# Kernel optimization log

Hardware: AMD Instinct MI355X
Metric: run time of the kernel (lower is better)

Reference implementation:

```python
import jax, jax.numpy as jnp
import numpy as np

B, S, N, U, E, L = 32, 32, 128, 64, 2, 2
N_STEPS = 3
NUM_CLASSES = 5


def setup_inputs() -> dict:
    key = jax.random.key(0)
    ks = jax.random.split(key, 10)
    input_seq = jax.random.normal(ks[0], (B, S, N * U), dtype=jnp.float32)
    seq_lengths = jax.random.randint(ks[1], (B,), 0, S)
    # per-edge-type adjacency, scaled ~row-stochastic for numerical sanity
    adjacency_matrix = jax.random.uniform(ks[2], (B, E, N, N), dtype=jnp.float32) / N
    sc = 1.0 / np.sqrt(U)
    W_msg = jax.random.normal(ks[3], (L, E, U, U), dtype=jnp.float32) * sc
    b_msg = jnp.zeros((L, U), dtype=jnp.float32)
    Wg = jax.random.normal(ks[4], (L, 3, U, U), dtype=jnp.float32) * sc  # gates from aggregated messages
    Ug = jax.random.normal(ks[5], (L, 3, U, U), dtype=jnp.float32) * sc  # gates from hidden state
    bg = jnp.zeros((L, 3, U), dtype=jnp.float32)
    fc_w = jax.random.normal(ks[6], (U, NUM_CLASSES), dtype=jnp.float32) * sc
    fc_b = jnp.zeros((NUM_CLASSES,), dtype=jnp.float32)
    return {
        "input_seq": input_seq, "seq_lengths": seq_lengths,
        "adjacency_matrix": adjacency_matrix,
        "W_msg": W_msg, "b_msg": b_msg, "Wg": Wg, "Ug": Ug, "bg": bg,
        "fc_w": fc_w, "fc_b": fc_b,
    }


def _ggnn_layer(h, A, W_msg_l, b_msg_l, Wg_l, Ug_l, bg_l):
    # h: [S,B,N,U], A: [B,E,N,N] (shared across timesteps)
    for _ in range(N_STEPS):
        # typed message passing: sum_e A_e @ h @ W_e
        a = jnp.einsum('benm,sbmu,euv->sbnv', A, h, W_msg_l) + b_msg_l
        g_a = jnp.einsum('sbnu,guv->gsbnv', a, Wg_l)  # [3,S,B,N,U]
        z = jax.nn.sigmoid(g_a[0] + h @ Ug_l[0] + bg_l[0])
        r = jax.nn.sigmoid(g_a[1] + h @ Ug_l[1] + bg_l[1])
        c = jnp.tanh(g_a[2] + (r * h) @ Ug_l[2] + bg_l[2])
        h = (1.0 - z) * h + z * c
    return h


def reference(input_seq, seq_lengths, adjacency_matrix, W_msg, b_msg, Wg, Ug, bg, fc_w, fc_b):
    # encoder: hidden state is NOT carried across timesteps in the original
    # (cell is called with current input only), so timesteps are vectorized.
    cur = input_seq.reshape(B, S, N, U).transpose(1, 0, 2, 3)  # [S,B,N,U]
    for l in range(L):
        cur = _ggnn_layer(cur, adjacency_matrix, W_msg[l], b_msg[l], Wg[l], Ug[l], bg[l])
    out = cur.transpose(1, 0, 2, 3)  # [B,S,N,U]
    idx = jnp.clip(seq_lengths - 1, 0, S - 1)
    last = out[jnp.arange(B), idx]  # [B,N,U] (last relevant timestep)
    # dropout is identity in eval mode
    logits = jax.nn.relu(last) @ fc_w + fc_b  # [B,N,C]
    return jnp.max(logits, axis=1)  # [B,C]
```

## Files before the change

### kernel.cpp

```cpp
#include <hip/hip_runtime.h>

#define B 32
#define S 32
#define N 128
#define U 64
#define E 2
#define NCLS 5


__device__ __forceinline__ float sigmoid_f(float x) {
    return __fdividef(1.f, 1.f + __expf(-x));
}
__device__ __forceinline__ float tanh_f(float x) {
    float t = __expf(-2.f * fabsf(x));
    float y = __fdividef(1.f - t, 1.f + t);
    return copysignf(y, x);
}
__device__ __forceinline__ float bcast(float v, int u) {
    return __uint_as_float(__builtin_amdgcn_readlane(__float_as_uint(v), u));
}

template <int FIRST, int LAST>
__global__ __launch_bounds__(512, 2) void k_step(
    const float* __restrict__ x, const int* __restrict__ lens,
    const float* __restrict__ hin, float* __restrict__ hout,
    const float* __restrict__ A, const float* __restrict__ Wmsg,
    const float* __restrict__ bmsg, const float* __restrict__ Wg,
    const float* __restrict__ Ug, const float* __restrict__ bg,
    const float* __restrict__ fcw, float* __restrict__ partial, int l) {
    __shared__ float sred[4][2][2][2][64];
    __shared__ float avred[4][2][2][64];
    __shared__ float gred[4][2][3][2][64];
    __shared__ float c2red[4][2][2][64];
    __shared__ float red[4 * NCLS];
    int tid = threadIdx.x;
    int wave = tid >> 6, lane = tid & 63;
    int g = wave & 3;
    int k = wave >> 2;
    int b = blockIdx.x >> 4;
    int j = blockIdx.x & 15;
    int n0 = __builtin_amdgcn_readfirstlane(j * 8 + g * 2);
    int u0 = __builtin_amdgcn_readfirstlane(k * 32);
    int m0 = __builtin_amdgcn_readfirstlane(k * 64);

    const float* __restrict__ hsrc;
    if (FIRST) {
        int idx = lens[b] - 1;
        idx = idx < 0 ? 0 : (idx > S - 1 ? S - 1 : idx);
        hsrc = x + (size_t)(b * S + idx) * N * U;
    } else {
        hsrc = hin + (size_t)b * N * U;
    }

    float hv0 = hsrc[(n0 + 0) * U + lane];
    float hv1 = hsrc[(n0 + 1) * U + lane];

    float s00 = 0.f, s01 = 0.f, s10 = 0.f, s11 = 0.f;
    {
        const float4* A00 = (const float4*)(A + (((size_t)b * E + 0) * N + n0 + 0) * N + m0);
        const float4* A10 = (const float4*)(A + (((size_t)b * E + 0) * N + n0 + 1) * N + m0);
        const float4* A01 = (const float4*)(A + (((size_t)b * E + 1) * N + n0 + 0) * N + m0);
        const float4* A11 = (const float4*)(A + (((size_t)b * E + 1) * N + n0 + 1) * N + m0);
#pragma unroll 8
        for (int m4 = 0; m4 < 16; ++m4) {
            float4 a00 = A00[m4], a10 = A10[m4], a01 = A01[m4], a11 = A11[m4];
            float q0 = hsrc[(m0 + m4 * 4 + 0) * U + lane];
            float q1 = hsrc[(m0 + m4 * 4 + 1) * U + lane];
            float q2 = hsrc[(m0 + m4 * 4 + 2) * U + lane];
            float q3 = hsrc[(m0 + m4 * 4 + 3) * U + lane];
            s00 = fmaf(a00.x, q0, s00); s00 = fmaf(a00.y, q1, s00);
            s00 = fmaf(a00.z, q2, s00); s00 = fmaf(a00.w, q3, s00);
            s10 = fmaf(a10.x, q0, s10); s10 = fmaf(a10.y, q1, s10);
            s10 = fmaf(a10.z, q2, s10); s10 = fmaf(a10.w, q3, s10);
            s01 = fmaf(a01.x, q0, s01); s01 = fmaf(a01.y, q1, s01);
            s01 = fmaf(a01.z, q2, s01); s01 = fmaf(a01.w, q3, s01);
            s11 = fmaf(a11.x, q0, s11); s11 = fmaf(a11.y, q1, s11);
            s11 = fmaf(a11.z, q2, s11); s11 = fmaf(a11.w, q3, s11);
        }
    }
    sred[g][k][0][0][lane] = s00;
    sred[g][k][0][1][lane] = s01;
    sred[g][k][1][0][lane] = s10;
    sred[g][k][1][1][lane] = s11;
    __syncthreads();
    s00 = sred[g][0][0][0][lane] + sred[g][1][0][0][lane];
    s01 = sred[g][0][0][1][lane] + sred[g][1][0][1][lane];
    s10 = sred[g][0][1][0][lane] + sred[g][1][1][0][lane];
    s11 = sred[g][0][1][1][lane] + sred[g][1][1][1][lane];

    float av0, av1;
    {
        float bm = (k == 0) ? bmsg[l * U + lane] : 0.f;
        av0 = bm; av1 = bm;
        const float* W0 = Wmsg + (size_t)(l * E + 0) * U * U + lane;
        const float* W1 = W0 + U * U;
#pragma unroll 16
        for (int uu = 0; uu < 32; ++uu) {
            int u = u0 + uu;
            float w = W0[u * U];
            av0 = fmaf(bcast(s00, u), w, av0);
            av1 = fmaf(bcast(s10, u), w, av1);
        }
#pragma unroll 16
        for (int uu = 0; uu < 32; ++uu) {
            int u = u0 + uu;
            float w = W1[u * U];
            av0 = fmaf(bcast(s01, u), w, av0);
            av1 = fmaf(bcast(s11, u), w, av1);
        }
    }
    avred[g][k][0][lane] = av0;
    avred[g][k][1][lane] = av1;
    __syncthreads();
    av0 = avred[g][0][0][lane] + avred[g][1][0][lane];
    av1 = avred[g][0][1][lane] + avred[g][1][1][lane];

    const float* Wg0 = Wg + (size_t)l * 3 * U * U + lane;
    const float* Wg1 = Wg0 + U * U;
    const float* Wg2 = Wg1 + U * U;
    const float* Ug0 = Ug + (size_t)l * 3 * U * U + lane;
    const float* Ug1 = Ug0 + U * U;
    const float* Ug2 = Ug1 + U * U;
    float accz0, accz1, accr0, accr1, accc0, accc1;
    {
        float bz = (k == 0) ? bg[(l * 3 + 0) * U + lane] : 0.f;
        float br = (k == 0) ? bg[(l * 3 + 1) * U + lane] : 0.f;
        float bcc = (k == 0) ? bg[(l * 3 + 2) * U + lane] : 0.f;
        accz0 = bz; accz1 = bz;
        accr0 = br; accr1 = br;
        accc0 = bcc; accc1 = bcc;
#pragma unroll 8
        for (int uu = 0; uu < 32; ++uu) {
            int u = u0 + uu;
            float w0 = Wg0[u * U], w1 = Wg1[u * U], w2 = Wg2[u * U];
            float g0 = Ug0[u * U], g1 = Ug1[u * U];
            float a0 = bcast(av0, u), a1 = bcast(av1, u);
            float h0 = bcast(hv0, u), h1 = bcast(hv1, u);
            accz0 = fmaf(a0, w0, accz0); accz0 = fmaf(h0, g0, accz0);
            accz1 = fmaf(a1, w0, accz1); accz1 = fmaf(h1, g0, accz1);
            accr0 = fmaf(a0, w1, accr0); accr0 = fmaf(h0, g1, accr0);
            accr1 = fmaf(a1, w1, accr1); accr1 = fmaf(h1, g1, accr1);
            accc0 = fmaf(a0, w2, accc0);
            accc1 = fmaf(a1, w2, accc1);
        }
    }
    gred[g][k][0][0][lane] = accz0; gred[g][k][0][1][lane] = accz1;
    gred[g][k][1][0][lane] = accr0; gred[g][k][1][1][lane] = accr1;
    gred[g][k][2][0][lane] = accc0; gred[g][k][2][1][lane] = accc1;
    __syncthreads();
    accz0 = gred[g][0][0][0][lane] + gred[g][1][0][0][lane];
    accz1 = gred[g][0][0][1][lane] + gred[g][1][0][1][lane];
    accr0 = gred[g][0][1][0][lane] + gred[g][1][1][0][lane];
    accr1 = gred[g][0][1][1][lane] + gred[g][1][1][1][lane];
    accc0 = gred[g][0][2][0][lane] + gred[g][1][2][0][lane];
    accc1 = gred[g][0][2][1][lane] + gred[g][1][2][1][lane];

    float rh0 = sigmoid_f(accr0) * hv0;
    float rh1 = sigmoid_f(accr1) * hv1;
    float c20 = 0.f, c21 = 0.f;
#pragma unroll 16
    for (int uu = 0; uu < 32; ++uu) {
        int u = u0 + uu;
        float g2 = Ug2[u * U];
        c20 = fmaf(bcast(rh0, u), g2, c20);
        c21 = fmaf(bcast(rh1, u), g2, c21);
    }
    c2red[g][k][0][lane] = c20;
    c2red[g][k][1][lane] = c21;
    __syncthreads();
    accc0 += c2red[g][0][0][lane] + c2red[g][1][0][lane];
    accc1 += c2red[g][0][1][lane] + c2red[g][1][1][lane];

    float zg0 = sigmoid_f(accz0), zg1 = sigmoid_f(accz1);
    float hn0 = (1.f - zg0) * hv0 + zg0 * tanh_f(accc0);
    float hn1 = (1.f - zg1) * hv1 + zg1 * tanh_f(accc1);

    if (!LAST) {
        if (k == 0) {
            hout[((size_t)b * N + n0 + 0) * U + lane] = hn0;
            hout[((size_t)b * N + n0 + 1) * U + lane] = hn1;
        }
    } else {
        float lg0[NCLS], lg1[NCLS];
        float rv0 = hn0 > 0.f ? hn0 : 0.f;
        float rv1 = hn1 > 0.f ? hn1 : 0.f;
#pragma unroll
        for (int c = 0; c < NCLS; c++) {
            float w = fcw[lane * NCLS + c];
            lg0[c] = rv0 * w;
            lg1[c] = rv1 * w;
        }
#pragma unroll
        for (int off = 32; off; off >>= 1) {
#pragma unroll
            for (int c = 0; c < NCLS; c++) {
                lg0[c] += __shfl_xor(lg0[c], off, 64);
                lg1[c] += __shfl_xor(lg1[c], off, 64);
            }
        }
        if (k == 0 && lane == 0) {
#pragma unroll
            for (int c = 0; c < NCLS; c++) red[g * NCLS + c] = fmaxf(lg0[c], lg1[c]);
        }
        __syncthreads();
        if (tid < NCLS) {
            float m = red[tid];
            for (int w = 1; w < 4; ++w) m = fmaxf(m, red[w * NCLS + tid]);
            partial[(size_t)(b * 16 + j) * NCLS + tid] = m;
        }
    }
}

__global__ void k_final(const float* __restrict__ partial, const float* __restrict__ fcb,
                        float* __restrict__ out) {
    int b = blockIdx.x, c = threadIdx.x;
    if (c < NCLS) {
        float m = -3.4e38f;
        for (int jj = 0; jj < 16; ++jj)
            m = fmaxf(m, partial[(size_t)(b * 16 + jj) * NCLS + c]);
        out[b * NCLS + c] = m + fcb[c];
    }
}

extern "C" void kernel_launch(void* const* d_in, const int* in_sizes, int n_in,
                              void* d_out, int out_size, void* d_ws, size_t ws_size,
                              hipStream_t stream) {
    const float* x    = (const float*)d_in[0];
    const int*   lens = (const int*)d_in[1];
    const float* A    = (const float*)d_in[2];
    const float* Wmsg = (const float*)d_in[3];
    const float* bmsg = (const float*)d_in[4];
    const float* Wg   = (const float*)d_in[5];
    const float* Ug   = (const float*)d_in[6];
    const float* bg   = (const float*)d_in[7];
    const float* fcw  = (const float*)d_in[8];
    const float* fcb  = (const float*)d_in[9];
    float* out = (float*)d_out;

    float* hA      = (float*)d_ws;
    float* hB      = hA + (size_t)B * N * U;
    float* partial = hB + (size_t)B * N * U;

    k_step<1, 0><<<B * 16, 512, 0, stream>>>(x, lens, nullptr, hA, A, Wmsg, bmsg, Wg, Ug, bg, fcw, partial, 0);
    k_step<0, 0><<<B * 16, 512, 0, stream>>>(x, lens, hA, hB, A, Wmsg, bmsg, Wg, Ug, bg, fcw, partial, 0);
    k_step<0, 0><<<B * 16, 512, 0, stream>>>(x, lens, hB, hA, A, Wmsg, bmsg, Wg, Ug, bg, fcw, partial, 0);
    k_step<0, 0><<<B * 16, 512, 0, stream>>>(x, lens, hA, hB, A, Wmsg, bmsg, Wg, Ug, bg, fcw, partial, 1);
    k_step<0, 0><<<B * 16, 512, 0, stream>>>(x, lens, hB, hA, A, Wmsg, bmsg, Wg, Ug, bg, fcw, partial, 1);
    k_step<0, 1><<<B * 16, 512, 0, stream>>>(x, lens, hA, hB, A, Wmsg, bmsg, Wg, Ug, bg, fcw, partial, 1);
    k_final<<<B, 64, 0, stream>>>(partial, fcb, out);
}
```

Measured before the change: 195.4 us.

## Stage layer weights in LDS and use 1024-thread blocks covering 16 nodes

Each block now copies the layer's message, gate and hidden-gate weight matrices into shared memory and reads them from there instead of global memory. The grid is halved to 256 blocks of 1024 threads, each handling 16 nodes, with the reduction buffers reused to cut shared-memory use. The change targets global/L2 weight-fetch latency in the inner matvec loops, at the cost of a ~128KB per-block staging copy on every launch and one block per CU.

```diff
diff --git a/kernel.cpp b/kernel.cpp
--- a/kernel.cpp
+++ b/kernel.cpp
@@ -21,27 +21,42 @@
 }
 
 template <int FIRST, int LAST>
-__global__ __launch_bounds__(512, 2) void k_step(
+__global__ __launch_bounds__(1024, 4) void k_step(
     const float* __restrict__ x, const int* __restrict__ lens,
     const float* __restrict__ hin, float* __restrict__ hout,
     const float* __restrict__ A, const float* __restrict__ Wmsg,
     const float* __restrict__ bmsg, const float* __restrict__ Wg,
     const float* __restrict__ Ug, const float* __restrict__ bg,
     const float* __restrict__ fcw, float* __restrict__ partial, int l) {
-    __shared__ float sred[4][2][2][2][64];
-    __shared__ float avred[4][2][2][64];
-    __shared__ float gred[4][2][3][2][64];
-    __shared__ float c2red[4][2][2][64];
-    __shared__ float red[4 * NCLS];
+    __shared__ float wms[E * U * U];
+    __shared__ float wgs[3 * U * U];
+    __shared__ float ugs[3 * U * U];
+    __shared__ float sA[8][2][2][2][64];
+    __shared__ float sB[8][2][2][64];
     int tid = threadIdx.x;
     int wave = tid >> 6, lane = tid & 63;
-    int g = wave & 3;
-    int k = wave >> 2;
-    int b = blockIdx.x >> 4;
-    int j = blockIdx.x & 15;
-    int n0 = __builtin_amdgcn_readfirstlane(j * 8 + g * 2);
+    int g = wave & 7;
+    int k = wave >> 3;
+    int b = blockIdx.x >> 3;
+    int j = blockIdx.x & 7;
+    int n0 = __builtin_amdgcn_readfirstlane(j * 16 + g * 2);
     int u0 = __builtin_amdgcn_readfirstlane(k * 32);
     int m0 = __builtin_amdgcn_readfirstlane(k * 64);
+
+    {
+        const float4* m4 = (const float4*)(Wmsg + (size_t)l * E * U * U);
+        float4* md = (float4*)wms;
+#pragma unroll
+        for (int i = 0; i < 2; ++i) md[tid + i * 1024] = m4[tid + i * 1024];
+        const float4* g4 = (const float4*)(Wg + (size_t)l * 3 * U * U);
+        float4* gd = (float4*)wgs;
+#pragma unroll
+        for (int i = 0; i < 3; ++i) gd[tid + i * 1024] = g4[tid + i * 1024];
+        const float4* u4 = (const float4*)(Ug + (size_t)l * 3 * U * U);
+        float4* ud = (float4*)ugs;
+#pragma unroll
+        for (int i = 0; i < 3; ++i) ud[tid + i * 1024] = u4[tid + i * 1024];
+    }
 
     const float* __restrict__ hsrc;
     if (FIRST) {
@@ -78,22 +93,22 @@
             s11 = fmaf(a11.z, q2, s11); s11 = fmaf(a11.w, q3, s11);
         }
     }
-    sred[g][k][0][0][lane] = s00;
-    sred[g][k][0][1][lane] = s01;
-    sred[g][k][1][0][lane] = s10;
-    sred[g][k][1][1][lane] = s11;
-    __syncthreads();
-    s00 = sred[g][0][0][0][lane] + sred[g][1][0][0][lane];
-    s01 = sred[g][0][0][1][lane] + sred[g][1][0][1][lane];
-    s10 = sred[g][0][1][0][lane] + sred[g][1][1][0][lane];
-    s11 = sred[g][0][1][1][lane] + sred[g][1][1][1][lane];
+    sA[g][k][0][0][lane] = s00;
+    sA[g][k][0][1][lane] = s01;
+    sA[g][k][1][0][lane] = s10;
+    sA[g][k][1][1][lane] = s11;
+    __syncthreads();
+    s00 = sA[g][0][0][0][lane] + sA[g][1][0][0][lane];
+    s01 = sA[g][0][0][1][lane] + sA[g][1][0][1][lane];
+    s10 = sA[g][0][1][0][lane] + sA[g][1][1][0][lane];
+    s11 = sA[g][0][1][1][lane] + sA[g][1][1][1][lane];
 
     float av0, av1;
     {
         float bm = (k == 0) ? bmsg[l * U + lane] : 0.f;
         av0 = bm; av1 = bm;
-        const float* W0 = Wmsg + (size_t)(l * E + 0) * U * U + lane;
-        const float* W1 = W0 + U * U;
+        const float* W0 = wms + lane;
+        const float* W1 = wms + U * U + lane;
 #pragma unroll 16
         for (int uu = 0; uu < 32; ++uu) {
             int u = u0 + uu;
@@ -109,18 +124,18 @@
             av1 = fmaf(bcast(s11, u), w, av1);
         }
     }
-    avred[g][k][0][lane] = av0;
-    avred[g][k][1][lane] = av1;
-    __syncthreads();
-    av0 = avred[g][0][0][lane] + avred[g][1][0][lane];
-    av1 = avred[g][0][1][lane] + avred[g][1][1][lane];
-
-    const float* Wg0 = Wg + (size_t)l * 3 * U * U + lane;
-    const float* Wg1 = Wg0 + U * U;
-    const float* Wg2 = Wg1 + U * U;
-    const float* Ug0 = Ug + (size_t)l * 3 * U * U + lane;
-    const float* Ug1 = Ug0 + U * U;
-    const float* Ug2 = Ug1 + U * U;
+    sB[g][k][0][lane] = av0;
+    sB[g][k][1][lane] = av1;
+    __syncthreads();
+    av0 = sB[g][0][0][lane] + sB[g][1][0][lane];
+    av1 = sB[g][0][1][lane] + sB[g][1][1][lane];
+
+    const float* Wg0 = wgs + lane;
+    const float* Wg1 = wgs + U * U + lane;
+    const float* Wg2 = wgs + 2 * U * U + lane;
+    const float* Ug0 = ugs + lane;
+    const float* Ug1 = ugs + U * U + lane;
+    const float* Ug2 = ugs + 2 * U * U + lane;
     float accz0, accz1, accr0, accr1, accc0, accc1;
     {
         float bz = (k == 0) ? bg[(l * 3 + 0) * U + lane] : 0.f;
@@ -144,16 +159,20 @@
             accc1 = fmaf(a1, w2, accc1);
         }
     }
-    gred[g][k][0][0][lane] = accz0; gred[g][k][0][1][lane] = accz1;
-    gred[g][k][1][0][lane] = accr0; gred[g][k][1][1][lane] = accr1;
-    gred[g][k][2][0][lane] = accc0; gred[g][k][2][1][lane] = accc1;
-    __syncthreads();
-    accz0 = gred[g][0][0][0][lane] + gred[g][1][0][0][lane];
-    accz1 = gred[g][0][0][1][lane] + gred[g][1][0][1][lane];
-    accr0 = gred[g][0][1][0][lane] + gred[g][1][1][0][lane];
-    accr1 = gred[g][0][1][1][lane] + gred[g][1][1][1][lane];
-    accc0 = gred[g][0][2][0][lane] + gred[g][1][2][0][lane];
-    accc1 = gred[g][0][2][1][lane] + gred[g][1][2][1][lane];
+    sA[g][k][0][0][lane] = accz0;
+    sA[g][k][0][1][lane] = accz1;
+    sA[g][k][1][0][lane] = accr0;
+    sA[g][k][1][1][lane] = accr1;
+    __syncthreads();
+    accz0 = sA[g][0][0][0][lane] + sA[g][1][0][0][lane];
+    accz1 = sA[g][0][0][1][lane] + sA[g][1][0][1][lane];
+    accr0 = sA[g][0][1][0][lane] + sA[g][1][1][0][lane];
+    accr1 = sA[g][0][1][1][lane] + sA[g][1][1][1][lane];
+    sB[g][k][0][lane] = accc0;
+    sB[g][k][1][lane] = accc1;
+    __syncthreads();
+    accc0 = sB[g][0][0][lane] + sB[g][1][0][lane];
+    accc1 = sB[g][0][1][lane] + sB[g][1][1][lane];
 
     float rh0 = sigmoid_f(accr0) * hv0;
     float rh1 = sigmoid_f(accr1) * hv1;
@@ -165,11 +184,11 @@
         c20 = fmaf(bcast(rh0, u), g2, c20);
         c21 = fmaf(bcast(rh1, u), g2, c21);
     }
-    c2red[g][k][0][lane] = c20;
-    c2red[g][k][1][lane] = c21;
-    __syncthreads();
-    accc0 += c2red[g][0][0][lane] + c2red[g][1][0][lane];
-    accc1 += c2red[g][0][1][lane] + c2red[g][1][1][lane];
+    sA[g][k][0][0][lane] = c20;
+    sA[g][k][0][1][lane] = c21;
+    __syncthreads();
+    accc0 += sA[g][0][0][0][lane] + sA[g][1][0][0][lane];
+    accc1 += sA[g][0][0][1][lane] + sA[g][1][0][1][lane];
 
     float zg0 = sigmoid_f(accz0), zg1 = sigmoid_f(accz1);
     float hn0 = (1.f - zg0) * hv0 + zg0 * tanh_f(accc0);
@@ -181,32 +200,36 @@
             hout[((size_t)b * N + n0 + 1) * U + lane] = hn1;
         }
     } else {
-        float lg0[NCLS], lg1[NCLS];
-        float rv0 = hn0 > 0.f ? hn0 : 0.f;
-        float rv1 = hn1 > 0.f ? hn1 : 0.f;
-#pragma unroll
-        for (int c = 0; c < NCLS; c++) {
-            float w = fcw[lane * NCLS + c];
-            lg0[c] = rv0 * w;
-            lg1[c] = rv1 * w;
-        }
-#pragma unroll
-        for (int off = 32; off; off >>= 1) {
+        float* red = &sB[0][0][0][0];
+        if (k == 0) {
+            float lg0[NCLS], lg1[NCLS];
+            float rv0 = hn0 > 0.f ? hn0 : 0.f;
+            float rv1 = hn1 > 0.f ? hn1 : 0.f;
 #pragma unroll
             for (int c = 0; c < NCLS; c++) {
-                lg0[c] += __shfl_xor(lg0[c], off, 64);
-                lg1[c] += __shfl_xor(lg1[c], off, 64);
+                float w = fcw[lane * NCLS + c];
+                lg0[c] = rv0 * w;
+                lg1[c] = rv1 * w;
             }
-        }
-        if (k == 0 && lane == 0) {
-#pragma unroll
-            for (int c = 0; c < NCLS; c++) red[g * NCLS + c] = fmaxf(lg0[c], lg1[c]);
+#pragma unroll
+            for (int off = 32; off; off >>= 1) {
+#pragma unroll
+                for (int c = 0; c < NCLS; c++) {
+                    lg0[c] += __shfl_xor(lg0[c], off, 64);
+                    lg1[c] += __shfl_xor(lg1[c], off, 64);
+                }
+            }
+            if (lane == 0) {
+#pragma unroll
+                for (int c = 0; c < NCLS; c++)
+                    red[g * NCLS + c] = fmaxf(lg0[c], lg1[c]);
+            }
         }
         __syncthreads();
         if (tid < NCLS) {
             float m = red[tid];
-            for (int w = 1; w < 4; ++w) m = fmaxf(m, red[w * NCLS + tid]);
-            partial[(size_t)(b * 16 + j) * NCLS + tid] = m;
+            for (int w = 1; w < 8; ++w) m = fmaxf(m, red[w * NCLS + tid]);
+            partial[(size_t)(b * 8 + j) * NCLS + tid] = m;
         }
     }
 }
@@ -216,8 +239,8 @@
     int b = blockIdx.x, c = threadIdx.x;
     if (c < NCLS) {
         float m = -3.4e38f;
-        for (int jj = 0; jj < 16; ++jj)
-            m = fmaxf(m, partial[(size_t)(b * 16 + jj) * NCLS + c]);
+        for (int jj = 0; jj < 8; ++jj)
+            m = fmaxf(m, partial[(size_t)(b * 8 + jj) * NCLS + c]);
         out[b * NCLS + c] = m + fcb[c];
     }
 }
@@ -241,11 +264,11 @@
     float* hB      = hA + (size_t)B * N * U;
     float* partial = hB + (size_t)B * N * U;
 
-    k_step<1, 0><<<B * 16, 512, 0, stream>>>(x, lens, nullptr, hA, A, Wmsg, bmsg, Wg, Ug, bg, fcw, partial, 0);
-    k_step<0, 0><<<B * 16, 512, 0, stream>>>(x, lens, hA, hB, A, Wmsg, bmsg, Wg, Ug, bg, fcw, partial, 0);
-    k_step<0, 0><<<B * 16, 512, 0, stream>>>(x, lens, hB, hA, A, Wmsg, bmsg, Wg, Ug, bg, fcw, partial, 0);
-    k_step<0, 0><<<B * 16, 512, 0, stream>>>(x, lens, hA, hB, A, Wmsg, bmsg, Wg, Ug, bg, fcw, partial, 1);
-    k_step<0, 0><<<B * 16, 512, 0, stream>>>(x, lens, hB, hA, A, Wmsg, bmsg, Wg, Ug, bg, fcw, partial, 1);
-    k_step<0, 1><<<B * 16, 512, 0, stream>>>(x, lens, hA, hB, A, Wmsg, bmsg, Wg, Ug, bg, fcw, partial, 1);
+    k_step<1, 0><<<B * 8, 1024, 0, stream>>>(x, lens, nullptr, hA, A, Wmsg, bmsg, Wg, Ug, bg, fcw, partial, 0);
+    k_step<0, 0><<<B * 8, 1024, 0, stream>>>(x, lens, hA, hB, A, Wmsg, bmsg, Wg, Ug, bg, fcw, partial, 0);
+    k_step<0, 0><<<B * 8, 1024, 0, stream>>>(x, lens, hB, hA, A, Wmsg, bmsg, Wg, Ug, bg, fcw, partial, 0);
+    k_step<0, 0><<<B * 8, 1024, 0, stream>>>(x, lens, hA, hB, A, Wmsg, bmsg, Wg, Ug, bg, fcw, partial, 1);
+    k_step<0, 0><<<B * 8, 1024, 0, stream>>>(x, lens, hB, hA, A, Wmsg, bmsg, Wg, Ug, bg, fcw, partial, 1);
+    k_step<0, 1><<<B * 8, 1024, 0, stream>>>(x, lens, hA, hB, A, Wmsg, bmsg, Wg, Ug, bg, fcw, partial, 1);
     k_final<<<B, 64, 0, stream>>>(partial, fcb, out);
 }
```

Measured after the change: 199.4 us. 2.0% more time.
